# Kernel tuning notes

Hardware: AMD Instinct MI355X
Metric: run time of the kernel (lower is better)

## Reference

```python
import jax, jax.numpy as jnp
import numpy as np

VOCAB, EMB, HID, OUT = 50000, 128, 256, 64
B, T = 256, 512


def setup_inputs() -> dict:
    key = jax.random.key(0)
    ks = jax.random.split(key, 9)
    # tokens in [1, VOCAB); then plant a single 0 (pad marker) per row at a
    # random position >= 1 so the original code's 'first zero - 1' index is valid
    x = jax.random.randint(ks[0], (B, T), 1, VOCAB)
    zero_pos = jax.random.randint(ks[1], (B,), 1, T)
    x = jax.vmap(lambda row, p: row.at[p].set(0))(x, zero_pos)
    s = 0.05
    emb = jax.random.normal(ks[2], (VOCAB, EMB), jnp.float32) * s
    W_ih = jax.random.normal(ks[3], (4 * HID, EMB), jnp.float32) * s
    W_hh = jax.random.normal(ks[4], (4 * HID, HID), jnp.float32) * s
    b_ih = jax.random.normal(ks[5], (4 * HID,), jnp.float32) * s
    b_hh = jax.random.normal(ks[6], (4 * HID,), jnp.float32) * s
    W_out = jax.random.normal(ks[7], (OUT, HID), jnp.float32) * s
    b_out = jax.random.normal(ks[8], (OUT,), jnp.float32) * s
    return dict(x=x, emb=emb, W_ih=W_ih, W_hh=W_hh, b_ih=b_ih, b_hh=b_hh,
                W_out=W_out, b_out=b_out)


def _lstm(xs, W_ih, W_hh, b_ih, b_hh):
    # xs: [T, B, E] time-major. PyTorch gate order: i, f, g, o.
    Tn, Bn, _ = xs.shape
    H = W_hh.shape[1]
    # precompute input contribution for all timesteps (one big GEMM)
    gx = jnp.einsum('tbe,ge->tbg', xs, W_ih) + b_ih + b_hh  # [T, B, 4H]

    def step(carry, g_x):
        h, c = carry
        g = g_x + h @ W_hh.T  # [B, 4H]
        i, f, gg, o = jnp.split(g, 4, axis=-1)
        c = jax.nn.sigmoid(f) * c + jax.nn.sigmoid(i) * jnp.tanh(gg)
        h = jax.nn.sigmoid(o) * jnp.tanh(c)
        return (h, c), h

    h0 = jnp.zeros((Bn, H), xs.dtype)
    _, hs = jax.lax.scan(step, (h0, h0), gx)
    return hs  # [T, B, H]


def reference(x, emb, W_ih, W_hh, b_ih, b_hh, W_out, b_out):
    Bn = x.shape[0]
    # last valid index = (first zero position) - 1, per sample
    idx = jnp.argmax(x == 0, axis=1) - 1  # [B]
    e = emb[x]                              # [B, T, E]
    hs = _lstm(e.transpose(1, 0, 2), W_ih, W_hh, b_ih, b_hh)  # [T, B, H]
    last = hs[idx, jnp.arange(Bn)]          # [B, H] gather last valid state
    logits = last @ W_out.T + b_out         # [B, OUT]
    return jax.nn.softmax(logits, axis=1)
```

## Files before the change

kernel.cpp:

```cpp
#include <hip/hip_runtime.h>
#include <stdint.h>

#define VOCAB 50000
#define EMBD  128
#define HID   256
#define G4    1024
#define BATCH 256
#define TSEQ  512
#define OUTD  64

typedef __attribute__((ext_vector_type(4))) float f32x4;
typedef __attribute__((ext_vector_type(8))) short short8;
typedef __attribute__((ext_vector_type(4))) unsigned short ushort4_t;
typedef __attribute__((ext_vector_type(8))) unsigned short ushort8_t;

__device__ inline unsigned short f2bf(float f) {
  unsigned u = __float_as_uint(f);
  u += 0x7fffu + ((u >> 16) & 1u);
  return (unsigned short)(u >> 16);
}
__device__ inline float bf2f(unsigned short u) {
  return __uint_as_float(((unsigned)u) << 16);
}
__device__ inline short8 pack2(f32x4 a, f32x4 b) {
  short8 r;
  r[0] = (short)f2bf(a[0]); r[1] = (short)f2bf(a[1]);
  r[2] = (short)f2bf(a[2]); r[3] = (short)f2bf(a[3]);
  r[4] = (short)f2bf(b[0]); r[5] = (short)f2bf(b[1]);
  r[6] = (short)f2bf(b[2]); r[7] = (short)f2bf(b[3]);
  return r;
}

__device__ inline void barrier_lds_only() {
  asm volatile("s_waitcnt lgkmcnt(0)\n\ts_barrier" ::: "memory");
}


__global__ __launch_bounds__(256) void wx_k1(
    const float* __restrict__ emb, const float* __restrict__ Wih,
    const float* __restrict__ bih, const float* __restrict__ bhh,
    unsigned short* __restrict__ Wx) {
  const int w1 = threadIdx.x >> 6, lane = threadIdx.x & 63;
  const int quad = lane >> 4, n = lane & 15;
  const int combo = blockIdx.y * 4 + w1;

  float bias[4];
  short8 bfr[4][4];
#pragma unroll
  for (int nt = 0; nt < 4; ++nt) {
    const int oj = nt * 256 + combo * 16 + n;
    bias[nt] = bih[oj] + bhh[oj];
#pragma unroll
    for (int kc = 0; kc < 4; ++kc) {
      const f32x4* wp = (const f32x4*)(Wih + (size_t)oj * EMBD + kc * 32 + quad * 8);
      bfr[nt][kc] = pack2(wp[0], wp[1]);
    }
  }

  for (int vt = 0; vt < 16; ++vt) {
    const int vb = blockIdx.x * 256 + vt * 16;
    if (vb >= VOCAB) break;
    short8 af[4];
#pragma unroll
    for (int kc = 0; kc < 4; ++kc) {
      const f32x4* ep = (const f32x4*)(emb + (size_t)(vb + n) * EMBD + kc * 32 + quad * 8);
      af[kc] = pack2(ep[0], ep[1]);
    }
    f32x4 acc[4];
#pragma unroll
    for (int nt = 0; nt < 4; ++nt) acc[nt] = (f32x4){0.f, 0.f, 0.f, 0.f};
#pragma unroll
    for (int kc = 0; kc < 4; ++kc)
#pragma unroll
      for (int nt = 0; nt < 4; ++nt)
        acc[nt] = __builtin_amdgcn_mfma_f32_16x16x32_bf16(af[kc], bfr[nt][kc], acc[nt], 0, 0, 0);
#pragma unroll
    for (int rr = 0; rr < 4; ++rr) {
      ushort4_t o;
#pragma unroll
      for (int nt = 0; nt < 4; ++nt) o[nt] = f2bf(acc[nt][rr] + bias[nt]);
      *(ushort4_t*)&Wx[(size_t)(vb + quad * 4 + rr) * G4 + (combo * 16 + n) * 4] = o;
    }
  }
}

__global__ __launch_bounds__(512, 2) void lstm_k2(
    const int* __restrict__ x, const float* __restrict__ Whh,
    const unsigned short* __restrict__ Wx,
    float* __restrict__ lastH) {
  const int group = blockIdx.x;
  const int rowbase = group * 4;
  const int tid = threadIdx.x;
  const int w = tid >> 6, lane = tid & 63;
  const int quad = lane >> 4, n = lane & 15;

  __shared__ __attribute__((aligned(16))) unsigned short h_lds[2][16][264];
  __shared__ __attribute__((aligned(16))) unsigned short wlds[8][2][4][2][64][8];
  __shared__ int xoff[4][TSEQ];
  __shared__ int zpos[4];

  if (tid < 4) zpos[tid] = 1 << 30;
  __syncthreads();
  for (int i = tid; i < 4 * TSEQ; i += 512) {
    const int row = i >> 9, tc = i & 511;
    const int tok = x[(size_t)(rowbase + row) * TSEQ + tc];
    if (tok == 0) atomicMin(&zpos[row], tc);
    xoff[row][tc] = tok * G4;
  }
  for (int i = tid; i < 2 * 16 * 264; i += 512) ((unsigned short*)h_lds)[i] = 0;

#pragma unroll
  for (int gl = 0; gl < 2; ++gl)
#pragma unroll
    for (int nt = 0; nt < 4; ++nt)
#pragma unroll
      for (int kcl = 0; kcl < 2; ++kcl) {
        const int oj = nt * 256 + w * 32 + 2 * n + gl;
        const f32x4* wp = (const f32x4*)(Whh + (size_t)oj * HID + (6 + kcl) * 32 + quad * 8);
        *(short8*)&wlds[w][gl][nt][kcl][lane][0] = pack2(wp[0], wp[1]);
      }

  short8 bfr[2][4][6];
#pragma unroll
  for (int gl = 0; gl < 2; ++gl)
#pragma unroll
    for (int nt = 0; nt < 4; ++nt) {
      const int oj = nt * 256 + w * 32 + 2 * n + gl;
      const float* wrow = Whh + (size_t)oj * HID;
#pragma unroll
      for (int kc = 0; kc < 6; ++kc) {
        const f32x4* wp = (const f32x4*)(wrow + kc * 32 + quad * 8);
        bfr[gl][nt][kc] = pack2(wp[0], wp[1]);
      }
    }

  float cst[2];
  cst[0] = 0.f; cst[1] = 0.f;

  __syncthreads();
  const int idxq = zpos[quad] - 1;

  const int ard = ((n & 3) == 0) ? (n * 528 + quad * 16) : 528;
  const int awr = quad * 2112 + (w * 32 + 2 * n) * 2;
  const unsigned lanewx = (unsigned)((w * 32 + 2 * n) * 4);
  char* hb = (char*)&h_lds[0][0][0];
  unsigned hoff = 0;

  ushort8_t wx8 = *(const ushort8_t*)(Wx + (size_t)(unsigned)xoff[quad][0] + lanewx);
  int toko = xoff[quad][1];

  for (int t = 0; t < TSEQ; ++t) {
    const int tnn = (t + 2 < TSEQ) ? (t + 2) : (TSEQ - 1);

    f32x4 acc[2][4];
#pragma unroll
    for (int gl = 0; gl < 2; ++gl)
#pragma unroll
      for (int nt = 0; nt < 4; ++nt)
        acc[gl][nt] = (f32x4){bf2f(wx8[gl * 4 + nt]), 0.f, 0.f, 0.f};

    wx8 = *(const ushort8_t*)(Wx + (size_t)(unsigned)toko + lanewx);
    const int tok_next = xoff[quad][tnn];

#pragma unroll
    for (int kc = 0; kc < 6; ++kc) {
      const short8 a = *(const short8*)(hb + hoff + ard + kc * 64);
#pragma unroll
      for (int gl = 0; gl < 2; ++gl)
#pragma unroll
        for (int nt = 0; nt < 4; ++nt)
          acc[gl][nt] = __builtin_amdgcn_mfma_f32_16x16x32_bf16(a, bfr[gl][nt][kc], acc[gl][nt], 0, 0, 0);
    }
#pragma unroll
    for (int kcl = 0; kcl < 2; ++kcl) {
      const short8 a = *(const short8*)(hb + hoff + ard + (6 + kcl) * 64);
#pragma unroll
      for (int gl = 0; gl < 2; ++gl)
#pragma unroll
        for (int nt = 0; nt < 4; ++nt) {
          const short8 b = *(const short8*)&wlds[w][gl][nt][kcl][lane][0];
          acc[gl][nt] = __builtin_amdgcn_mfma_f32_16x16x32_bf16(a, b, acc[gl][nt], 0, 0, 0);
        }
    }

    toko = tok_next;

    float hv2[2];
#pragma unroll
    for (int gl = 0; gl < 2; ++gl) {
      const float ei = __expf(-acc[gl][0][0]), ef = __expf(-acc[gl][1][0]);
      const float eg2 = __expf(2.0f * acc[gl][2][0]), eo = __expf(-acc[gl][3][0]);
      const float r1 = __builtin_amdgcn_rcpf(1.0f + ef);
      const float r2 = __builtin_amdgcn_rcpf((1.0f + ei) * (eg2 + 1.0f));
      const float ci = cst[gl] * r1 + (eg2 - 1.0f) * r2;
      cst[gl] = ci;
      const float ec2 = __expf(2.0f * ci);
      const float r3 = __builtin_amdgcn_rcpf((1.0f + eo) * (ec2 + 1.0f));
      hv2[gl] = (ec2 - 1.0f) * r3;
    }
    const unsigned pk = (unsigned)f2bf(hv2[0]) | ((unsigned)f2bf(hv2[1]) << 16);
    *(unsigned*)(hb + (hoff ^ 8448u) + awr) = pk;

    if (t == idxq) {
      const size_t o0 = (size_t)(rowbase + quad) * HID + (w * 32 + 2 * n);
      lastH[o0] = hv2[0];
      lastH[o0 + 1] = hv2[1];
    }

    hoff ^= 8448u;
    barrier_lds_only();
  }
}

__global__ __launch_bounds__(64) void head_k3(
    const float* __restrict__ lastH, const float* __restrict__ Wout,
    const float* __restrict__ bout, float* __restrict__ out) {
  const int b = blockIdx.x, j = threadIdx.x;
  const f32x4* hv = (const f32x4*)(lastH + (size_t)b * HID);
  const f32x4* wv = (const f32x4*)(Wout + (size_t)j * HID);
  float acc = bout[j];
#pragma unroll 8
  for (int k = 0; k < HID / 4; ++k) {
    const f32x4 a = hv[k], ww = wv[k];
    acc += a[0] * ww[0] + a[1] * ww[1] + a[2] * ww[2] + a[3] * ww[3];
  }
  float m = acc;
  for (int s = 32; s > 0; s >>= 1) m = fmaxf(m, __shfl_xor(m, s, 64));
  const float e = __expf(acc - m);
  float ssum = e;
  for (int s = 32; s > 0; s >>= 1) ssum += __shfl_xor(ssum, s, 64);
  out[(size_t)b * OUTD + j] = e / ssum;
}

extern "C" void kernel_launch(void* const* d_in, const int* in_sizes, int n_in,
                              void* d_out, int out_size, void* d_ws, size_t ws_size,
                              hipStream_t stream) {
  const int*   x    = (const int*)d_in[0];
  const float* emb  = (const float*)d_in[1];
  const float* Wih  = (const float*)d_in[2];
  const float* Whh  = (const float*)d_in[3];
  const float* bih  = (const float*)d_in[4];
  const float* bhh  = (const float*)d_in[5];
  const float* Wout = (const float*)d_in[6];
  const float* bout = (const float*)d_in[7];
  float* out = (float*)d_out;

  char* ws = (char*)d_ws;
  unsigned short* Wx = (unsigned short*)ws;
  float* lastH = (float*)(ws + 102400000);

  hipLaunchKernelGGL(wx_k1, dim3(196, 4), dim3(256), 0, stream,
                     emb, Wih, bih, bhh, Wx);
  hipLaunchKernelGGL(lstm_k2, dim3(64), dim3(512), 0, stream,
                     x, Whh, Wx, lastH);
  hipLaunchKernelGGL(head_k3, dim3(BATCH), dim3(OUTD), 0, stream,
                     lastH, Wout, bout, out);
}
```

Measured before the change: 1.036 ms.

## Fuse output head into LSTM kernel and share embedding tiles via LDS in wx kernel

Removes the separate head kernel: the last valid hidden state is kept in registers, written to LDS after the recurrence, and each LSTM block computes the output projection and softmax for its 4 rows. This drops one kernel launch and the global round trip of lastH. In the Wx precompute kernel, the embedding tile is now loaded once per block, with each wave loading a quarter, into a double-buffered LDS tile. Previously every wave reloaded the full tile from global memory. The cost is an extra __syncthreads per vocab tile and a predicated select inside the recurrence loop.

Measured after the change: 1.034 ms. Within noise of the previous version (-0.3%).

```diff
diff --git a/kernel.cpp b/kernel.cpp
--- a/kernel.cpp
+++ b/kernel.cpp
@@ -44,6 +44,8 @@
   const int quad = lane >> 4, n = lane & 15;
   const int combo = blockIdx.y * 4 + w1;
 
+  __shared__ __attribute__((aligned(16))) unsigned short etile[2][16][136];
+
   float bias[4];
   short8 bfr[4][4];
 #pragma unroll
@@ -57,15 +59,25 @@
     }
   }
 
+  {
+    const int vb0 = blockIdx.x * 256;
+    const f32x4* ep = (const f32x4*)(emb + (size_t)(vb0 + n) * EMBD + w1 * 32 + quad * 8);
+    *(short8*)&etile[0][n][w1 * 32 + quad * 8] = pack2(ep[0], ep[1]);
+  }
+
   for (int vt = 0; vt < 16; ++vt) {
     const int vb = blockIdx.x * 256 + vt * 16;
     if (vb >= VOCAB) break;
+    __syncthreads();
+    const int vbn = vb + 16;
+    if (vt < 15 && vbn < VOCAB) {
+      const f32x4* ep = (const f32x4*)(emb + (size_t)(vbn + n) * EMBD + w1 * 32 + quad * 8);
+      *(short8*)&etile[(vt + 1) & 1][n][w1 * 32 + quad * 8] = pack2(ep[0], ep[1]);
+    }
     short8 af[4];
 #pragma unroll
-    for (int kc = 0; kc < 4; ++kc) {
-      const f32x4* ep = (const f32x4*)(emb + (size_t)(vb + n) * EMBD + kc * 32 + quad * 8);
-      af[kc] = pack2(ep[0], ep[1]);
-    }
+    for (int kc = 0; kc < 4; ++kc)
+      af[kc] = *(const short8*)&etile[vt & 1][n][kc * 32 + quad * 8];
     f32x4 acc[4];
 #pragma unroll
     for (int nt = 0; nt < 4; ++nt) acc[nt] = (f32x4){0.f, 0.f, 0.f, 0.f};
@@ -87,7 +99,8 @@
 __global__ __launch_bounds__(512, 2) void lstm_k2(
     const int* __restrict__ x, const float* __restrict__ Whh,
     const unsigned short* __restrict__ Wx,
-    float* __restrict__ lastH) {
+    const float* __restrict__ Wout, const float* __restrict__ bout,
+    float* __restrict__ out) {
   const int group = blockIdx.x;
   const int rowbase = group * 4;
   const int tid = threadIdx.x;
@@ -134,8 +147,9 @@
       }
     }
 
-  float cst[2];
+  float cst[2], lastreg[2];
   cst[0] = 0.f; cst[1] = 0.f;
+  lastreg[0] = 0.f; lastreg[1] = 0.f;
 
   __syncthreads();
   const int idxq = zpos[quad] - 1;
@@ -197,39 +211,41 @@
       const float ec2 = __expf(2.0f * ci);
       const float r3 = __builtin_amdgcn_rcpf((1.0f + eo) * (ec2 + 1.0f));
       hv2[gl] = (ec2 - 1.0f) * r3;
+      lastreg[gl] = (t == idxq) ? hv2[gl] : lastreg[gl];
     }
     const unsigned pk = (unsigned)f2bf(hv2[0]) | ((unsigned)f2bf(hv2[1]) << 16);
     *(unsigned*)(hb + (hoff ^ 8448u) + awr) = pk;
 
-    if (t == idxq) {
-      const size_t o0 = (size_t)(rowbase + quad) * HID + (w * 32 + 2 * n);
-      lastH[o0] = hv2[0];
-      lastH[o0 + 1] = hv2[1];
-    }
-
     hoff ^= 8448u;
     barrier_lds_only();
   }
-}
-
-__global__ __launch_bounds__(64) void head_k3(
-    const float* __restrict__ lastH, const float* __restrict__ Wout,
-    const float* __restrict__ bout, float* __restrict__ out) {
-  const int b = blockIdx.x, j = threadIdx.x;
-  const f32x4* hv = (const f32x4*)(lastH + (size_t)b * HID);
-  const f32x4* wv = (const f32x4*)(Wout + (size_t)j * HID);
-  float acc = bout[j];
+
+  __syncthreads();
+  float* hfin = (float*)&h_lds[0][0][0];
+  {
+    const int u0 = w * 32 + 2 * n;
+    hfin[quad * HID + u0] = lastreg[0];
+    hfin[quad * HID + u0 + 1] = lastreg[1];
+  }
+  __syncthreads();
+  if (tid < 256) {
+    const int r = tid >> 6, j = tid & 63;
+    const float* hr = hfin + r * HID;
+    const f32x4* wv = (const f32x4*)(Wout + (size_t)j * HID);
+    float acc = bout[j];
 #pragma unroll 8
-  for (int k = 0; k < HID / 4; ++k) {
-    const f32x4 a = hv[k], ww = wv[k];
-    acc += a[0] * ww[0] + a[1] * ww[1] + a[2] * ww[2] + a[3] * ww[3];
-  }
-  float m = acc;
-  for (int s = 32; s > 0; s >>= 1) m = fmaxf(m, __shfl_xor(m, s, 64));
-  const float e = __expf(acc - m);
-  float ssum = e;
-  for (int s = 32; s > 0; s >>= 1) ssum += __shfl_xor(ssum, s, 64);
-  out[(size_t)b * OUTD + j] = e / ssum;
+    for (int k = 0; k < HID / 4; ++k) {
+      const f32x4 a = *(const f32x4*)(hr + 4 * k);
+      const f32x4 ww = wv[k];
+      acc += a[0] * ww[0] + a[1] * ww[1] + a[2] * ww[2] + a[3] * ww[3];
+    }
+    float m = acc;
+    for (int s = 32; s > 0; s >>= 1) m = fmaxf(m, __shfl_xor(m, s, 64));
+    const float e = __expf(acc - m);
+    float ssum = e;
+    for (int s = 32; s > 0; s >>= 1) ssum += __shfl_xor(ssum, s, 64);
+    out[(size_t)(rowbase + r) * OUTD + j] = e / ssum;
+  }
 }
 
 extern "C" void kernel_launch(void* const* d_in, const int* in_sizes, int n_in,
@@ -247,12 +263,9 @@
 
   char* ws = (char*)d_ws;
   unsigned short* Wx = (unsigned short*)ws;
-  float* lastH = (float*)(ws + 102400000);
 
   hipLaunchKernelGGL(wx_k1, dim3(196, 4), dim3(256), 0, stream,
                      emb, Wih, bih, bhh, Wx);
   hipLaunchKernelGGL(lstm_k2, dim3(64), dim3(512), 0, stream,
-                     x, Whh, Wx, lastH);
-  hipLaunchKernelGGL(head_k3, dim3(BATCH), dim3(OUTD), 0, stream,
-                     lastH, Wout, bout, out);
-}
+                     x, Whh, Wx, Wout, bout, out);
+}
```
